# Optimization experiments

Measured on AMD Instinct MI355X. Metric: run time of the kernel, lower is better.

Reference implementation:

```python
import jax, jax.numpy as jnp
import numpy as np

B, S, D = 2, 2048, 1024
H = 16
DH = D // H


def setup_inputs() -> dict:
    key = jax.random.key(0)
    ks = jax.random.split(key, 6)
    scale = 1.0 / np.sqrt(D)
    x = jax.random.normal(ks[0], (B, S, D), dtype=jnp.float32)
    Wq = jax.random.normal(ks[1], (D, D), dtype=jnp.float32) * scale
    Wk = jax.random.normal(ks[2], (D, D), dtype=jnp.float32) * scale
    Wv = jax.random.normal(ks[3], (D, D), dtype=jnp.float32) * scale
    Wo = jax.random.normal(ks[4], (D, D), dtype=jnp.float32) * scale
    bo = jax.random.normal(ks[5], (D,), dtype=jnp.float32) * 0.01
    return {"x": x, "Wq": Wq, "Wk": Wk, "Wv": Wv, "Wo": Wo, "bo": bo}


def reference(x, Wq, Wk, Wv, Wo, bo):
    b, t, _ = x.shape
    # project and split heads: [b, h, t, dh]
    q = (x @ Wq).reshape(b, t, H, DH).transpose(0, 2, 1, 3)
    k = (x @ Wk).reshape(b, t, H, DH).transpose(0, 2, 1, 3)
    v = (x @ Wv).reshape(b, t, H, DH).transpose(0, 2, 1, 3)
    scores = jnp.einsum('bhqd,bhkd->bhqk', q, k)
    causal = jnp.triu(jnp.ones((t, t), dtype=bool), k=1)
    scores = jnp.where(causal, -jnp.inf, scores)
    attn = jax.nn.softmax(scores / np.sqrt(DH), axis=-1)
    ctx = jnp.einsum('bhqk,bhkd->bhqd', attn, v)
    ctx = ctx.transpose(0, 2, 1, 3).reshape(b, t, D)
    return ctx @ Wo + bo
```

## Files before the change

kernel.cpp:

```cpp
#include <hip/hip_runtime.h>
#include <hip/hip_bf16.h>

#define B 2
#define S 2048
#define D 1024
#define NH 16
#define DH 64
#define M (B*S)
#define BQ 128
#define BK 64
#define KSCALE 0.18033688011112042f

typedef __hip_bfloat16 bf16;
typedef __attribute__((ext_vector_type(8))) short frag_ab;
typedef __attribute__((ext_vector_type(4))) float frag_cd;
typedef unsigned long long ull;

__device__ __forceinline__ void gload_lds16(const bf16* g, bf16* l) {
    __builtin_amdgcn_global_load_lds((const __attribute__((address_space(1))) unsigned int*)g,
                                     (__attribute__((address_space(3))) unsigned int*)l,
                                     16, 0, 0);
}

__global__ __launch_bounds__(256) void cvt_x(const float* __restrict__ x, bf16* __restrict__ xb) {
    const int i = (blockIdx.x * 256 + threadIdx.x) * 4;
    const float4 v = *(const float4*)(x + i);
    __align__(8) bf16 t[4] = {__float2bfloat16(v.x), __float2bfloat16(v.y),
                              __float2bfloat16(v.z), __float2bfloat16(v.w)};
    *(ull*)(xb + i) = *(const ull*)t;
}

__global__ __launch_bounds__(256) void cvt_wT(const float* __restrict__ W0, const float* __restrict__ W1,
                                              const float* __restrict__ W2, const float* __restrict__ W3,
                                              bf16* __restrict__ T0, bf16* __restrict__ T1,
                                              bf16* __restrict__ T2, bf16* __restrict__ T3) {
    const float* src; bf16* dst;
    switch (blockIdx.z) {
        case 0: src = W0; dst = T0; break;
        case 1: src = W1; dst = T1; break;
        case 2: src = W2; dst = T2; break;
        default: src = W3; dst = T3; break;
    }
    __shared__ float t[32][33];
    const int tx = threadIdx.x & 31, ty = threadIdx.x >> 5;
    const int c0 = blockIdx.x * 32, r0 = blockIdx.y * 32;
#pragma unroll
    for (int i = 0; i < 4; i++)
        t[ty + 8 * i][tx] = src[(size_t)(r0 + ty + 8 * i) * D + c0 + tx];
    __syncthreads();
#pragma unroll
    for (int i = 0; i < 4; i++)
        dst[(size_t)(c0 + ty + 8 * i) * D + r0 + tx] = __float2bfloat16(t[tx][ty + 8 * i]);
}

__global__ __launch_bounds__(256) void gemm_qkv_all(const bf16* __restrict__ A, const bf16* __restrict__ Bt,
                                                    bf16* __restrict__ Qb, bf16* __restrict__ Kb,
                                                    bf16* __restrict__ Vt_g) {
    __shared__ __align__(16) bf16 As[128 * BK];
    __shared__ __align__(16) bf16 Bs[128 * BK];
    const int tid = threadIdx.x, wave = tid >> 6, lane = tid & 63;
    const int r16 = lane & 15, quad = lane >> 4;
    const int row0 = blockIdx.y * 128;
    const int col0 = blockIdx.x * 128;
    const int wm = (wave & 1) * 64, wn = (wave >> 1) * 64;

    frag_cd acc[4][4];
#pragma unroll
    for (int mt = 0; mt < 4; mt++)
#pragma unroll
        for (int nt = 0; nt < 4; nt++) acc[mt][nt] = frag_cd{0.f, 0.f, 0.f, 0.f};

    for (int k0 = 0; k0 < D; k0 += BK) {
        __syncthreads();
#pragma unroll
        for (int j = 0; j < 4; j++) {
            const int s = wave * 256 + j * 64 + lane;
            const int r = s >> 3;
            const int c = (s ^ r) & 7;
            gload_lds16(A  + (size_t)(row0 + r) * D + k0 + c * 8, &As[(wave * 256 + j * 64) * 8]);
            gload_lds16(Bt + (size_t)(col0 + r) * D + k0 + c * 8, &Bs[(wave * 256 + j * 64) * 8]);
        }
        __syncthreads();

        frag_ab af[4][2], bf[4][2];
#pragma unroll
        for (int mt = 0; mt < 4; mt++) {
            const int row = wm + mt * 16 + r16;
#pragma unroll
            for (int ks = 0; ks < 2; ks++)
                af[mt][ks] = *(const frag_ab*)&As[row * 64 + (((ks * 4 + quad) ^ (row & 7)) * 8)];
        }
#pragma unroll
        for (int nt = 0; nt < 4; nt++) {
            const int row = wn + nt * 16 + r16;
#pragma unroll
            for (int ks = 0; ks < 2; ks++)
                bf[nt][ks] = *(const frag_ab*)&Bs[row * 64 + (((ks * 4 + quad) ^ (row & 7)) * 8)];
        }
#pragma unroll
        for (int mt = 0; mt < 4; mt++)
#pragma unroll
            for (int nt = 0; nt < 4; nt++)
#pragma unroll
                for (int ks = 0; ks < 2; ks++)
                    acc[mt][nt] = __builtin_amdgcn_mfma_f32_16x16x32_bf16(
                        af[mt][ks], bf[nt][ks], acc[mt][nt], 0, 0, 0);
    }

    const int third = col0 >> 10;
    if (third < 2) {
        bf16* Out = (third == 0) ? Qb : Kb;
#pragma unroll
        for (int mt = 0; mt < 4; mt++)
#pragma unroll
            for (int nt = 0; nt < 4; nt++) {
                const int cl = (col0 + wn + nt * 16 + r16) & 1023;
#pragma unroll
                for (int rg = 0; rg < 4; rg++) {
                    const int row = row0 + wm + mt * 16 + quad * 4 + rg;
                    Out[(size_t)row * D + cl] = __float2bfloat16(acc[mt][nt][rg]);
                }
            }
    } else {
        const int bb = row0 >> 11;
        const int sb0 = (row0 & 2047) + wm;
#pragma unroll
        for (int mt = 0; mt < 4; mt++)
#pragma unroll
            for (int nt = 0; nt < 4; nt++) {
                const int c  = (col0 + wn + nt * 16 + r16) - 2048;
                const int hh = c >> 6, dl = c & 63;
                const int sb = sb0 + mt * 16 + quad * 4;
                __align__(8) bf16 t4[4];
#pragma unroll
                for (int rg = 0; rg < 4; rg++) t4[rg] = __float2bfloat16(acc[mt][nt][rg]);
                *(ull*)(Vt_g + (((size_t)bb * 16 + hh) * 64 + dl) * S + sb) = *(const ull*)t4;
            }
    }
}

__global__ __launch_bounds__(256) void attn_mfma(const bf16* __restrict__ Q,
                                                 const bf16* __restrict__ K,
                                                 const bf16* __restrict__ Vg,
                                                 bf16* __restrict__ Ctx) {
    __shared__ __align__(16) bf16 Ks[2][BK * DH];
    __shared__ __align__(16) bf16 Vt[2][BK * DH];
    __shared__ __align__(16) bf16 Qs[BQ * DH];
    bf16* Ps = Qs;

    const int tid = threadIdx.x, wave = tid >> 6, lane = tid & 63;
    const int r16 = lane & 15, quad = lane >> 4;
    const int bh = blockIdx.x, jy = blockIdx.y;
    const int qt = (jy < 8) ? jy : 23 - jy;
    const int b = bh >> 4, h = bh & 15;
    const size_t base  = (size_t)b * S * D + (size_t)h * DH;
    const size_t vbase = (size_t)bh * DH * S;
    const int q0 = qt * BQ;
    const int qwave = q0 + wave * 32;
    const int nkt = 2 * qt + 2;

#pragma unroll
    for (int j = 0; j < 4; j++) {
        const int s = wave * 256 + j * 64 + lane;
        const int r = s >> 3;
        const int c = (s ^ r) & 7;
        gload_lds16(Q + base + (size_t)(q0 + r) * D + c * 8, &Qs[(wave * 256 + j * 64) * 8]);
    }
#pragma unroll
    for (int j = 0; j < 2; j++) {
        const int s = wave * 128 + j * 64 + lane;
        const int r = s >> 3;
        const int c = (s ^ r) & 7;
        gload_lds16(K  + base  + (size_t)r * D + c * 8, &Ks[0][(wave * 128 + j * 64) * 8]);
        gload_lds16(Vg + vbase + (size_t)r * S + c * 8, &Vt[0][(wave * 128 + j * 64) * 8]);
    }
    __syncthreads();

    frag_ab qf[2][2];
#pragma unroll
    for (int nq = 0; nq < 2; nq++)
#pragma unroll
        for (int ks = 0; ks < 2; ks++) {
            const int row = wave * 32 + nq * 16 + r16;
            qf[nq][ks] = *(const frag_ab*)&Qs[row * 64 + (((ks * 4 + quad) ^ (row & 7)) * 8)];
        }

    float mrun[2] = {-1e30f, -1e30f}, lrun[2] = {0.f, 0.f};
    frag_cd Oacc[2][4];
#pragma unroll
    for (int mq = 0; mq < 2; mq++)
#pragma unroll
        for (int nd = 0; nd < 4; nd++) Oacc[mq][nd] = frag_cd{0.f, 0.f, 0.f, 0.f};

    for (int kt = 0; kt < nkt; kt++) {
        const int k0  = kt * BK;
        const int cur = kt & 1;

        if (kt + 1 < nkt) {
            const int kn = k0 + BK;
#pragma unroll
            for (int j = 0; j < 2; j++) {
                const int s = wave * 128 + j * 64 + lane;
                const int r = s >> 3;
                const int c = (s ^ r) & 7;
                gload_lds16(K  + base  + (size_t)(kn + r) * D + c * 8,
                            &Ks[cur ^ 1][(wave * 128 + j * 64) * 8]);
                gload_lds16(Vg + vbase + (size_t)r * S + kn + c * 8,
                            &Vt[cur ^ 1][(wave * 128 + j * 64) * 8]);
            }
        }

        if (k0 <= qwave + 31) {
            frag_ab ka[4][2];
#pragma unroll
            for (int mk = 0; mk < 4; mk++) {
                const int row = mk * 16 + r16;
#pragma unroll
                for (int ks = 0; ks < 2; ks++)
                    ka[mk][ks] = *(const frag_ab*)&Ks[cur][row * 64 + (((ks * 4 + quad) ^ (row & 7)) * 8)];
            }
            const bool domask = (k0 + BK - 1 > qwave);

#pragma unroll
            for (int nq = 0; nq < 2; nq++) {
                frag_cd Sc[4];
#pragma unroll
                for (int mk = 0; mk < 4; mk++) {
                    Sc[mk] = frag_cd{0.f, 0.f, 0.f, 0.f};
#pragma unroll
                    for (int ks = 0; ks < 2; ks++)
                        Sc[mk] = __builtin_amdgcn_mfma_f32_16x16x32_bf16(
                            ka[mk][ks], qf[nq][ks], Sc[mk], 0, 0, 0);
                }
                const int qg = q0 + wave * 32 + nq * 16 + r16;
                float mx = -1e30f;
#pragma unroll
                for (int mk = 0; mk < 4; mk++)
#pragma unroll
                    for (int rg = 0; rg < 4; rg++) {
                        float sv = Sc[mk][rg] * KSCALE;
                        if (domask) {
                            const int keyg = k0 + mk * 16 + quad * 4 + rg;
                            sv = (keyg <= qg) ? sv : -1e30f;
                        }
                        Sc[mk][rg] = sv;
                        mx = fmaxf(mx, sv);
                    }
                mx = fmaxf(mx, __shfl_xor(mx, 16, 64));
                mx = fmaxf(mx, __shfl_xor(mx, 32, 64));
                const float mnew  = fmaxf(mrun[nq], mx);
                const float alpha = __builtin_amdgcn_exp2f(mrun[nq] - mnew);
                mrun[nq] = mnew;
                float rs = 0.f;
#pragma unroll
                for (int mk = 0; mk < 4; mk++)
#pragma unroll
                    for (int rg = 0; rg < 4; rg++) {
                        const float p = __builtin_amdgcn_exp2f(Sc[mk][rg] - mnew);
                        Sc[mk][rg] = p;
                        rs += p;
                    }
                rs += __shfl_xor(rs, 16, 64);
                rs += __shfl_xor(rs, 32, 64);
                lrun[nq] = lrun[nq] * alpha + rs;

                const int qrow = wave * 32 + nq * 16 + r16;
#pragma unroll
                for (int mk = 0; mk < 4; mk++) {
                    __align__(8) bf16 t4[4];
#pragma unroll
                    for (int rg = 0; rg < 4; rg++) t4[rg] = __float2bfloat16(Sc[mk][rg]);
                    const int g = (mk * 4 + quad) ^ r16;
                    *(ull*)&Ps[qrow * 64 + g * 4] = *(const ull*)t4;
                }
#pragma unroll
                for (int nd = 0; nd < 4; nd++)
#pragma unroll
                    for (int rg = 0; rg < 4; rg++) Oacc[nq][nd][rg] *= alpha;
            }

            frag_ab pa[2][2], vb[4][2];
#pragma unroll
            for (int mq = 0; mq < 2; mq++) {
                const int row = wave * 32 + mq * 16 + r16;
#pragma unroll
                for (int ks = 0; ks < 2; ks++) {
                    const int gb = ks * 8 + quad * 2;
                    union { ull u[2]; frag_ab f; } t;
                    t.u[0] = *(const ull*)&Ps[row * 64 + ((gb    ) ^ r16) * 4];
                    t.u[1] = *(const ull*)&Ps[row * 64 + ((gb + 1) ^ r16) * 4];
                    pa[mq][ks] = t.f;
                }
            }
#pragma unroll
            for (int nd = 0; nd < 4; nd++) {
                const int row = nd * 16 + r16;
#pragma unroll
                for (int ks = 0; ks < 2; ks++)
                    vb[nd][ks] = *(const frag_ab*)&Vt[cur][row * 64 + (((ks * 4 + quad) ^ (row & 7)) * 8)];
            }
#pragma unroll
            for (int mq = 0; mq < 2; mq++)
#pragma unroll
                for (int nd = 0; nd < 4; nd++)
#pragma unroll
                    for (int ks = 0; ks < 2; ks++)
                        Oacc[mq][nd] = __builtin_amdgcn_mfma_f32_16x16x32_bf16(
                            vb[nd][ks], pa[mq][ks], Oacc[mq][nd], 0, 0, 0);
        }

        __syncthreads();
    }

#pragma unroll
    for (int mq = 0; mq < 2; mq++) {
        const float invl = 1.f / lrun[mq];
        const int qg = q0 + wave * 32 + mq * 16 + r16;
#pragma unroll
        for (int nd = 0; nd < 4; nd++) {
            __align__(8) bf16 t4[4];
#pragma unroll
            for (int rg = 0; rg < 4; rg++)
                t4[rg] = __float2bfloat16(Oacc[mq][nd][rg] * invl);
            *(ull*)(Ctx + base + (size_t)qg * D + nd * 16 + quad * 4) = *(const ull*)t4;
        }
    }
}

__global__ __launch_bounds__(256) void gemm_out64(const bf16* __restrict__ A, const bf16* __restrict__ Bt,
                                                  const float* __restrict__ bias, float* __restrict__ Out) {
    __shared__ __align__(16) bf16 As[64 * BK];
    __shared__ __align__(16) bf16 Bs[128 * BK];
    const int tid = threadIdx.x, wave = tid >> 6, lane = tid & 63;
    const int r16 = lane & 15, quad = lane >> 4;
    const int row0 = blockIdx.y * 64;
    const int col0 = blockIdx.x * 128;
    const int wm = (wave & 1) * 32, wn = (wave >> 1) * 64;

    frag_cd acc[2][4];
#pragma unroll
    for (int mt = 0; mt < 2; mt++)
#pragma unroll
        for (int nt = 0; nt < 4; nt++) acc[mt][nt] = frag_cd{0.f, 0.f, 0.f, 0.f};

    for (int k0 = 0; k0 < D; k0 += BK) {
        __syncthreads();
#pragma unroll
        for (int j = 0; j < 2; j++) {
            const int s = wave * 128 + j * 64 + lane;
            const int r = s >> 3;
            const int c = (s ^ r) & 7;
            gload_lds16(A + (size_t)(row0 + r) * D + k0 + c * 8, &As[(wave * 128 + j * 64) * 8]);
        }
#pragma unroll
        for (int j = 0; j < 4; j++) {
            const int s = wave * 256 + j * 64 + lane;
            const int r = s >> 3;
            const int c = (s ^ r) & 7;
            gload_lds16(Bt + (size_t)(col0 + r) * D + k0 + c * 8, &Bs[(wave * 256 + j * 64) * 8]);
        }
        __syncthreads();

        frag_ab af[2][2], bf[4][2];
#pragma unroll
        for (int mt = 0; mt < 2; mt++) {
            const int row = wm + mt * 16 + r16;
#pragma unroll
            for (int ks = 0; ks < 2; ks++)
                af[mt][ks] = *(const frag_ab*)&As[row * 64 + (((ks * 4 + quad) ^ (row & 7)) * 8)];
        }
#pragma unroll
        for (int nt = 0; nt < 4; nt++) {
            const int row = wn + nt * 16 + r16;
#pragma unroll
            for (int ks = 0; ks < 2; ks++)
                bf[nt][ks] = *(const frag_ab*)&Bs[row * 64 + (((ks * 4 + quad) ^ (row & 7)) * 8)];
        }
#pragma unroll
        for (int mt = 0; mt < 2; mt++)
#pragma unroll
            for (int nt = 0; nt < 4; nt++)
#pragma unroll
                for (int ks = 0; ks < 2; ks++)
                    acc[mt][nt] = __builtin_amdgcn_mfma_f32_16x16x32_bf16(
                        af[mt][ks], bf[nt][ks], acc[mt][nt], 0, 0, 0);
    }

#pragma unroll
    for (int mt = 0; mt < 2; mt++)
#pragma unroll
        for (int nt = 0; nt < 4; nt++) {
            const int col = col0 + wn + nt * 16 + r16;
            const float bv = bias[col];
#pragma unroll
            for (int rg = 0; rg < 4; rg++) {
                const int row = row0 + wm + mt * 16 + quad * 4 + rg;
                Out[(size_t)row * D + col] = acc[mt][nt][rg] + bv;
            }
        }
}

extern "C" void kernel_launch(void* const* d_in, const int* in_sizes, int n_in,
                              void* d_out, int out_size, void* d_ws, size_t ws_size,
                              hipStream_t stream) {
    const float* x  = (const float*)d_in[0];
    const float* Wq = (const float*)d_in[1];
    const float* Wk = (const float*)d_in[2];
    const float* Wv = (const float*)d_in[3];
    const float* Wo = (const float*)d_in[4];
    const float* bo = (const float*)d_in[5];
    float* out = (float*)d_out;

    bf16* xb    = (bf16*)d_ws;
    bf16* WqkvT = xb    + (size_t)M * D;
    bf16* WoT   = WqkvT + (size_t)3 * D * D;
    bf16* Qb    = WoT   + (size_t)D * D;
    bf16* Kb    = Qb    + (size_t)M * D;
    bf16* Vt_g  = Kb    + (size_t)M * D;
    bf16* Ctxb  = Vt_g  + (size_t)M * D;

    cvt_x<<<(M * D) / 1024, 256, 0, stream>>>(x, xb);
    cvt_wT<<<dim3(32, 32, 4), 256, 0, stream>>>(Wq, Wk, Wv, Wo,
                                                WqkvT, WqkvT + (size_t)D * D,
                                                WqkvT + (size_t)2 * D * D, WoT);
    gemm_qkv_all<<<dim3(24, 32), 256, 0, stream>>>(xb, WqkvT, Qb, Kb, Vt_g);
    attn_mfma<<<dim3(B * NH, S / BQ), 256, 0, stream>>>(Qb, Kb, Vt_g, Ctxb);
    gemm_out64<<<dim3(8, 64), 256, 0, stream>>>(Ctxb, WoT, bo, out);
}
```

Measured before the change: 187.5 us.

## Process key tiles in pairs per barrier and fold softmax scale into Q

The attention loop now stages two 64-key K/V tiles per double-buffer slot and processes both before each barrier and prefetch, halving the number of __syncthreads and prefetch rounds. The softmax scale (including the log2e factor) is applied to Q in the projection epilogue, which removes a per-score multiply from the attention inner loop. LDS use per block rises to about 80KB, which may lower the number of resident blocks per CU. Pre-scaling Q before bf16 rounding also shifts rounding slightly.

```diff
diff --git a/kernel.cpp b/kernel.cpp
--- a/kernel.cpp
+++ b/kernel.cpp
@@ -110,6 +110,7 @@
     const int third = col0 >> 10;
     if (third < 2) {
         bf16* Out = (third == 0) ? Qb : Kb;
+        const float sc = (third == 0) ? KSCALE : 1.f;
 #pragma unroll
         for (int mt = 0; mt < 4; mt++)
 #pragma unroll
@@ -118,7 +119,7 @@
 #pragma unroll
                 for (int rg = 0; rg < 4; rg++) {
                     const int row = row0 + wm + mt * 16 + quad * 4 + rg;
-                    Out[(size_t)row * D + cl] = __float2bfloat16(acc[mt][nt][rg]);
+                    Out[(size_t)row * D + cl] = __float2bfloat16(acc[mt][nt][rg] * sc);
                 }
             }
     } else {
@@ -143,8 +144,8 @@
                                                  const bf16* __restrict__ K,
                                                  const bf16* __restrict__ Vg,
                                                  bf16* __restrict__ Ctx) {
-    __shared__ __align__(16) bf16 Ks[2][BK * DH];
-    __shared__ __align__(16) bf16 Vt[2][BK * DH];
+    __shared__ __align__(16) bf16 Ks[2][2][BK * DH];
+    __shared__ __align__(16) bf16 Vt[2][2][BK * DH];
     __shared__ __align__(16) bf16 Qs[BQ * DH];
     bf16* Ps = Qs;
 
@@ -157,7 +158,7 @@
     const size_t vbase = (size_t)bh * DH * S;
     const int q0 = qt * BQ;
     const int qwave = q0 + wave * 32;
-    const int nkt = 2 * qt + 2;
+    const int npair = qt + 1;
 
 #pragma unroll
     for (int j = 0; j < 4; j++) {
@@ -171,8 +172,13 @@
         const int s = wave * 128 + j * 64 + lane;
         const int r = s >> 3;
         const int c = (s ^ r) & 7;
-        gload_lds16(K  + base  + (size_t)r * D + c * 8, &Ks[0][(wave * 128 + j * 64) * 8]);
-        gload_lds16(Vg + vbase + (size_t)r * S + c * 8, &Vt[0][(wave * 128 + j * 64) * 8]);
+#pragma unroll
+        for (int sub = 0; sub < 2; sub++) {
+            gload_lds16(K  + base  + (size_t)(sub * 64 + r) * D + c * 8,
+                        &Ks[0][sub][(wave * 128 + j * 64) * 8]);
+            gload_lds16(Vg + vbase + (size_t)r * S + sub * 64 + c * 8,
+                        &Vt[0][sub][(wave * 128 + j * 64) * 8]);
+        }
     }
     __syncthreads();
 
@@ -192,32 +198,38 @@
 #pragma unroll
         for (int nd = 0; nd < 4; nd++) Oacc[mq][nd] = frag_cd{0.f, 0.f, 0.f, 0.f};
 
-    for (int kt = 0; kt < nkt; kt++) {
-        const int k0  = kt * BK;
-        const int cur = kt & 1;
-
-        if (kt + 1 < nkt) {
-            const int kn = k0 + BK;
+    for (int p = 0; p < npair; p++) {
+        const int cur = p & 1;
+
+        if (p + 1 < npair) {
+            const int kn = (2 * p + 2) * BK;
 #pragma unroll
             for (int j = 0; j < 2; j++) {
                 const int s = wave * 128 + j * 64 + lane;
                 const int r = s >> 3;
                 const int c = (s ^ r) & 7;
-                gload_lds16(K  + base  + (size_t)(kn + r) * D + c * 8,
-                            &Ks[cur ^ 1][(wave * 128 + j * 64) * 8]);
-                gload_lds16(Vg + vbase + (size_t)r * S + kn + c * 8,
-                            &Vt[cur ^ 1][(wave * 128 + j * 64) * 8]);
-            }
-        }
-
-        if (k0 <= qwave + 31) {
+#pragma unroll
+                for (int sub = 0; sub < 2; sub++) {
+                    gload_lds16(K  + base  + (size_t)(kn + sub * 64 + r) * D + c * 8,
+                                &Ks[cur ^ 1][sub][(wave * 128 + j * 64) * 8]);
+                    gload_lds16(Vg + vbase + (size_t)r * S + kn + sub * 64 + c * 8,
+                                &Vt[cur ^ 1][sub][(wave * 128 + j * 64) * 8]);
+                }
+            }
+        }
+
+#pragma unroll
+        for (int sub = 0; sub < 2; sub++) {
+            const int k0 = (2 * p + sub) * BK;
+            if (k0 > qwave + 31) continue;
+
             frag_ab ka[4][2];
 #pragma unroll
             for (int mk = 0; mk < 4; mk++) {
                 const int row = mk * 16 + r16;
 #pragma unroll
                 for (int ks = 0; ks < 2; ks++)
-                    ka[mk][ks] = *(const frag_ab*)&Ks[cur][row * 64 + (((ks * 4 + quad) ^ (row & 7)) * 8)];
+                    ka[mk][ks] = *(const frag_ab*)&Ks[cur][sub][row * 64 + (((ks * 4 + quad) ^ (row & 7)) * 8)];
             }
             const bool domask = (k0 + BK - 1 > qwave);
 
@@ -238,7 +250,7 @@
                 for (int mk = 0; mk < 4; mk++)
 #pragma unroll
                     for (int rg = 0; rg < 4; rg++) {
-                        float sv = Sc[mk][rg] * KSCALE;
+                        float sv = Sc[mk][rg];
                         if (domask) {
                             const int keyg = k0 + mk * 16 + quad * 4 + rg;
                             sv = (keyg <= qg) ? sv : -1e30f;
@@ -256,9 +268,9 @@
                 for (int mk = 0; mk < 4; mk++)
 #pragma unroll
                     for (int rg = 0; rg < 4; rg++) {
-                        const float p = __builtin_amdgcn_exp2f(Sc[mk][rg] - mnew);
-                        Sc[mk][rg] = p;
-                        rs += p;
+                        const float pv = __builtin_amdgcn_exp2f(Sc[mk][rg] - mnew);
+                        Sc[mk][rg] = pv;
+                        rs += pv;
                     }
                 rs += __shfl_xor(rs, 16, 64);
                 rs += __shfl_xor(rs, 32, 64);
@@ -297,7 +309,7 @@
                 const int row = nd * 16 + r16;
 #pragma unroll
                 for (int ks = 0; ks < 2; ks++)
-                    vb[nd][ks] = *(const frag_ab*)&Vt[cur][row * 64 + (((ks * 4 + quad) ^ (row & 7)) * 8)];
+                    vb[nd][ks] = *(const frag_ab*)&Vt[cur][sub][row * 64 + (((ks * 4 + quad) ^ (row & 7)) * 8)];
             }
 #pragma unroll
             for (int mq = 0; mq < 2; mq++)
```

Measured after the change: 186.7 us. No clear change (-0.4%).

## Double-buffer LDS in both GEMMs, shrink QKV tile, fold softmax scale into Q

Applied to the files above, without the earlier changes.

Both projection GEMMs now use double-buffered LDS tiles, so the next K-slice is fetched while MFMAs run on the current one, with a single barrier per iteration. The QKV GEMM tile drops from 128x128 to 64x128, doubling its grid to give more blocks for the GPU's CUs. The attention score scale is applied once when Q is written, removing a multiply per score in the attention inner loop. The costs are twice the LDS per GEMM block, fewer MFMAs per loaded byte in the QKV GEMM, and rounding of the pre-scaled Q to bf16.

```diff
diff --git a/kernel.cpp b/kernel.cpp
--- a/kernel.cpp
+++ b/kernel.cpp
@@ -56,76 +56,101 @@
 __global__ __launch_bounds__(256) void gemm_qkv_all(const bf16* __restrict__ A, const bf16* __restrict__ Bt,
                                                     bf16* __restrict__ Qb, bf16* __restrict__ Kb,
                                                     bf16* __restrict__ Vt_g) {
-    __shared__ __align__(16) bf16 As[128 * BK];
-    __shared__ __align__(16) bf16 Bs[128 * BK];
+    __shared__ __align__(16) bf16 As[2][64 * BK];
+    __shared__ __align__(16) bf16 Bs[2][128 * BK];
     const int tid = threadIdx.x, wave = tid >> 6, lane = tid & 63;
     const int r16 = lane & 15, quad = lane >> 4;
-    const int row0 = blockIdx.y * 128;
+    const int row0 = blockIdx.y * 64;
     const int col0 = blockIdx.x * 128;
-    const int wm = (wave & 1) * 64, wn = (wave >> 1) * 64;
-
-    frag_cd acc[4][4];
-#pragma unroll
-    for (int mt = 0; mt < 4; mt++)
+    const int wm = (wave & 1) * 32, wn = (wave >> 1) * 64;
+
+    frag_cd acc[2][4];
+#pragma unroll
+    for (int mt = 0; mt < 2; mt++)
 #pragma unroll
         for (int nt = 0; nt < 4; nt++) acc[mt][nt] = frag_cd{0.f, 0.f, 0.f, 0.f};
 
-    for (int k0 = 0; k0 < D; k0 += BK) {
-        __syncthreads();
-#pragma unroll
-        for (int j = 0; j < 4; j++) {
-            const int s = wave * 256 + j * 64 + lane;
-            const int r = s >> 3;
-            const int c = (s ^ r) & 7;
-            gload_lds16(A  + (size_t)(row0 + r) * D + k0 + c * 8, &As[(wave * 256 + j * 64) * 8]);
-            gload_lds16(Bt + (size_t)(col0 + r) * D + k0 + c * 8, &Bs[(wave * 256 + j * 64) * 8]);
-        }
-        __syncthreads();
-
-        frag_ab af[4][2], bf[4][2];
-#pragma unroll
-        for (int mt = 0; mt < 4; mt++) {
+#pragma unroll
+    for (int j = 0; j < 2; j++) {
+        const int s = wave * 128 + j * 64 + lane;
+        const int r = s >> 3, c = (s ^ r) & 7;
+        gload_lds16(A + (size_t)(row0 + r) * D + c * 8, &As[0][(wave * 128 + j * 64) * 8]);
+    }
+#pragma unroll
+    for (int j = 0; j < 4; j++) {
+        const int s = wave * 256 + j * 64 + lane;
+        const int r = s >> 3, c = (s ^ r) & 7;
+        gload_lds16(Bt + (size_t)(col0 + r) * D + c * 8, &Bs[0][(wave * 256 + j * 64) * 8]);
+    }
+    __syncthreads();
+
+    for (int kt = 0; kt < D / BK; kt++) {
+        const int cur = kt & 1;
+        if (kt + 1 < D / BK) {
+            const int kn = (kt + 1) * BK;
+#pragma unroll
+            for (int j = 0; j < 2; j++) {
+                const int s = wave * 128 + j * 64 + lane;
+                const int r = s >> 3, c = (s ^ r) & 7;
+                gload_lds16(A + (size_t)(row0 + r) * D + kn + c * 8,
+                            &As[cur ^ 1][(wave * 128 + j * 64) * 8]);
+            }
+#pragma unroll
+            for (int j = 0; j < 4; j++) {
+                const int s = wave * 256 + j * 64 + lane;
+                const int r = s >> 3, c = (s ^ r) & 7;
+                gload_lds16(Bt + (size_t)(col0 + r) * D + kn + c * 8,
+                            &Bs[cur ^ 1][(wave * 256 + j * 64) * 8]);
+            }
+        }
+
+        frag_ab af[2][2], bf[4][2];
+#pragma unroll
+        for (int mt = 0; mt < 2; mt++) {
             const int row = wm + mt * 16 + r16;
 #pragma unroll
             for (int ks = 0; ks < 2; ks++)
-                af[mt][ks] = *(const frag_ab*)&As[row * 64 + (((ks * 4 + quad) ^ (row & 7)) * 8)];
+                af[mt][ks] = *(const frag_ab*)&As[cur][row * 64 + (((ks * 4 + quad) ^ (row & 7)) * 8)];
         }
 #pragma unroll
         for (int nt = 0; nt < 4; nt++) {
             const int row = wn + nt * 16 + r16;
 #pragma unroll
             for (int ks = 0; ks < 2; ks++)
-                bf[nt][ks] = *(const frag_ab*)&Bs[row * 64 + (((ks * 4 + quad) ^ (row & 7)) * 8)];
-        }
-#pragma unroll
-        for (int mt = 0; mt < 4; mt++)
+                bf[nt][ks] = *(const frag_ab*)&Bs[cur][row * 64 + (((ks * 4 + quad) ^ (row & 7)) * 8)];
+        }
+#pragma unroll
+        for (int mt = 0; mt < 2; mt++)
 #pragma unroll
             for (int nt = 0; nt < 4; nt++)
 #pragma unroll
                 for (int ks = 0; ks < 2; ks++)
                     acc[mt][nt] = __builtin_amdgcn_mfma_f32_16x16x32_bf16(
                         af[mt][ks], bf[nt][ks], acc[mt][nt], 0, 0, 0);
+
+        __syncthreads();
     }
 
     const int third = col0 >> 10;
     if (third < 2) {
         bf16* Out = (third == 0) ? Qb : Kb;
-#pragma unroll
-        for (int mt = 0; mt < 4; mt++)
+        const float sc = (third == 0) ? KSCALE : 1.f;
+#pragma unroll
+        for (int mt = 0; mt < 2; mt++)
 #pragma unroll
             for (int nt = 0; nt < 4; nt++) {
                 const int cl = (col0 + wn + nt * 16 + r16) & 1023;
 #pragma unroll
                 for (int rg = 0; rg < 4; rg++) {
                     const int row = row0 + wm + mt * 16 + quad * 4 + rg;
-                    Out[(size_t)row * D + cl] = __float2bfloat16(acc[mt][nt][rg]);
+                    Out[(size_t)row * D + cl] = __float2bfloat16(acc[mt][nt][rg] * sc);
                 }
             }
     } else {
         const int bb = row0 >> 11;
         const int sb0 = (row0 & 2047) + wm;
 #pragma unroll
-        for (int mt = 0; mt < 4; mt++)
+        for (int mt = 0; mt < 2; mt++)
 #pragma unroll
             for (int nt = 0; nt < 4; nt++) {
                 const int c  = (col0 + wn + nt * 16 + r16) - 2048;
@@ -162,15 +187,13 @@
 #pragma unroll
     for (int j = 0; j < 4; j++) {
         const int s = wave * 256 + j * 64 + lane;
-        const int r = s >> 3;
-        const int c = (s ^ r) & 7;
+        const int r = s >> 3, c = (s ^ r) & 7;
         gload_lds16(Q + base + (size_t)(q0 + r) * D + c * 8, &Qs[(wave * 256 + j * 64) * 8]);
     }
 #pragma unroll
     for (int j = 0; j < 2; j++) {
         const int s = wave * 128 + j * 64 + lane;
-        const int r = s >> 3;
-        const int c = (s ^ r) & 7;
+        const int r = s >> 3, c = (s ^ r) & 7;
         gload_lds16(K  + base  + (size_t)r * D + c * 8, &Ks[0][(wave * 128 + j * 64) * 8]);
         gload_lds16(Vg + vbase + (size_t)r * S + c * 8, &Vt[0][(wave * 128 + j * 64) * 8]);
     }
@@ -201,8 +224,7 @@
 #pragma unroll
             for (int j = 0; j < 2; j++) {
                 const int s = wave * 128 + j * 64 + lane;
-                const int r = s >> 3;
-                const int c = (s ^ r) & 7;
+                const int r = s >> 3, c = (s ^ r) & 7;
                 gload_lds16(K  + base  + (size_t)(kn + r) * D + c * 8,
                             &Ks[cur ^ 1][(wave * 128 + j * 64) * 8]);
                 gload_lds16(Vg + vbase + (size_t)r * S + kn + c * 8,
@@ -238,7 +260,7 @@
                 for (int mk = 0; mk < 4; mk++)
 #pragma unroll
                     for (int rg = 0; rg < 4; rg++) {
-                        float sv = Sc[mk][rg] * KSCALE;
+                        float sv = Sc[mk][rg];
                         if (domask) {
                             const int keyg = k0 + mk * 16 + quad * 4 + rg;
                             sv = (keyg <= qg) ? sv : -1e30f;
@@ -256,9 +278,9 @@
                 for (int mk = 0; mk < 4; mk++)
 #pragma unroll
                     for (int rg = 0; rg < 4; rg++) {
-                        const float p = __builtin_amdgcn_exp2f(Sc[mk][rg] - mnew);
-                        Sc[mk][rg] = p;
-                        rs += p;
+                        const float pv = __builtin_amdgcn_exp2f(Sc[mk][rg] - mnew);
+                        Sc[mk][rg] = pv;
+                        rs += pv;
                     }
                 rs += __shfl_xor(rs, 16, 64);
                 rs += __shfl_xor(rs, 32, 64);
@@ -329,8 +351,8 @@
 
 __global__ __launch_bounds__(256) void gemm_out64(const bf16* __restrict__ A, const bf16* __restrict__ Bt,
                                                   const float* __restrict__ bias, float* __restrict__ Out) {
-    __shared__ __align__(16) bf16 As[64 * BK];
-    __shared__ __align__(16) bf16 Bs[128 * BK];
+    __shared__ __align__(16) bf16 As[2][64 * BK];
+    __shared__ __align__(16) bf16 Bs[2][128 * BK];
     const int tid = threadIdx.x, wave = tid >> 6, lane = tid & 63;
     const int r16 = lane & 15, quad = lane >> 4;
     const int row0 = blockIdx.y * 64;
@@ -343,23 +365,39 @@
 #pragma unroll
         for (int nt = 0; nt < 4; nt++) acc[mt][nt] = frag_cd{0.f, 0.f, 0.f, 0.f};
 
-    for (int k0 = 0; k0 < D; k0 += BK) {
-        __syncthreads();
-#pragma unroll
-        for (int j = 0; j < 2; j++) {
-            const int s = wave * 128 + j * 64 + lane;
-            const int r = s >> 3;
-            const int c = (s ^ r) & 7;
-            gload_lds16(A + (size_t)(row0 + r) * D + k0 + c * 8, &As[(wave * 128 + j * 64) * 8]);
-        }
-#pragma unroll
-        for (int j = 0; j < 4; j++) {
-            const int s = wave * 256 + j * 64 + lane;
-            const int r = s >> 3;
-            const int c = (s ^ r) & 7;
-            gload_lds16(Bt + (size_t)(col0 + r) * D + k0 + c * 8, &Bs[(wave * 256 + j * 64) * 8]);
-        }
-        __syncthreads();
+#pragma unroll
+    for (int j = 0; j < 2; j++) {
+        const int s = wave * 128 + j * 64 + lane;
+        const int r = s >> 3, c = (s ^ r) & 7;
+        gload_lds16(A + (size_t)(row0 + r) * D + c * 8, &As[0][(wave * 128 + j * 64) * 8]);
+    }
+#pragma unroll
+    for (int j = 0; j < 4; j++) {
+        const int s = wave * 256 + j * 64 + lane;
+        const int r = s >> 3, c = (s ^ r) & 7;
+        gload_lds16(Bt + (size_t)(col0 + r) * D + c * 8, &Bs[0][(wave * 256 + j * 64) * 8]);
+    }
+    __syncthreads();
+
+    for (int kt = 0; kt < D / BK; kt++) {
+        const int cur = kt & 1;
+        if (kt + 1 < D / BK) {
+            const int kn = (kt + 1) * BK;
+#pragma unroll
+            for (int j = 0; j < 2; j++) {
+                const int s = wave * 128 + j * 64 + lane;
+                const int r = s >> 3, c = (s ^ r) & 7;
+                gload_lds16(A + (size_t)(row0 + r) * D + kn + c * 8,
+                            &As[cur ^ 1][(wave * 128 + j * 64) * 8]);
+            }
+#pragma unroll
+            for (int j = 0; j < 4; j++) {
+                const int s = wave * 256 + j * 64 + lane;
+                const int r = s >> 3, c = (s ^ r) & 7;
+                gload_lds16(Bt + (size_t)(col0 + r) * D + kn + c * 8,
+                            &Bs[cur ^ 1][(wave * 256 + j * 64) * 8]);
+            }
+        }
 
         frag_ab af[2][2], bf[4][2];
 #pragma unroll
@@ -367,14 +405,14 @@
             const int row = wm + mt * 16 + r16;
 #pragma unroll
             for (int ks = 0; ks < 2; ks++)
-                af[mt][ks] = *(const frag_ab*)&As[row * 64 + (((ks * 4 + quad) ^ (row & 7)) * 8)];
+                af[mt][ks] = *(const frag_ab*)&As[cur][row * 64 + (((ks * 4 + quad) ^ (row & 7)) * 8)];
         }
 #pragma unroll
         for (int nt = 0; nt < 4; nt++) {
             const int row = wn + nt * 16 + r16;
 #pragma unroll
             for (int ks = 0; ks < 2; ks++)
-                bf[nt][ks] = *(const frag_ab*)&Bs[row * 64 + (((ks * 4 + quad) ^ (row & 7)) * 8)];
+                bf[nt][ks] = *(const frag_ab*)&Bs[cur][row * 64 + (((ks * 4 + quad) ^ (row & 7)) * 8)];
         }
 #pragma unroll
         for (int mt = 0; mt < 2; mt++)
@@ -384,6 +422,8 @@
                 for (int ks = 0; ks < 2; ks++)
                     acc[mt][nt] = __builtin_amdgcn_mfma_f32_16x16x32_bf16(
                         af[mt][ks], bf[nt][ks], acc[mt][nt], 0, 0, 0);
+
+        __syncthreads();
     }
 
 #pragma unroll
@@ -423,7 +463,7 @@
     cvt_wT<<<dim3(32, 32, 4), 256, 0, stream>>>(Wq, Wk, Wv, Wo,
                                                 WqkvT, WqkvT + (size_t)D * D,
                                                 WqkvT + (size_t)2 * D * D, WoT);
-    gemm_qkv_all<<<dim3(24, 32), 256, 0, stream>>>(xb, WqkvT, Qb, Kb, Vt_g);
+    gemm_qkv_all<<<dim3(24, 64), 256, 0, stream>>>(xb, WqkvT, Qb, Kb, Vt_g);
     attn_mfma<<<dim3(B * NH, S / BQ), 256, 0, stream>>>(Qb, Kb, Vt_g, Ctxb);
     gemm_out64<<<dim3(8, 64), 256, 0, stream>>>(Ctxb, WoT, bo, out);
 }
```

New measurement: 199.3 us. +6.3%, slower.

## Halve attention query tile to 64 rows and fold softmax scale into Q

Applied to the files above, without the earlier changes.

Shrinks the attention query tile from 128 to 64 rows, so each wave owns 16 query rows instead of 32. This doubles the number of blocks and cuts per-wave register state, which should help occupancy and load balance across CUs. The softmax scale is now applied to Q in the projection epilogue, removing a multiply per score element. The cost is that each K/V tile is reused by half as many queries, so K/V traffic per query rises; the launch grid presumably also changes in hidden code.

```diff
diff --git a/kernel.cpp b/kernel.cpp
--- a/kernel.cpp
+++ b/kernel.cpp
@@ -7,7 +7,7 @@
 #define NH 16
 #define DH 64
 #define M (B*S)
-#define BQ 128
+#define BQ 64
 #define BK 64
 #define KSCALE 0.18033688011112042f
 
@@ -110,6 +110,7 @@
     const int third = col0 >> 10;
     if (third < 2) {
         bf16* Out = (third == 0) ? Qb : Kb;
+        const float sc = (third == 0) ? KSCALE : 1.f;
 #pragma unroll
         for (int mt = 0; mt < 4; mt++)
 #pragma unroll
@@ -118,7 +119,7 @@
 #pragma unroll
                 for (int rg = 0; rg < 4; rg++) {
                     const int row = row0 + wm + mt * 16 + quad * 4 + rg;
-                    Out[(size_t)row * D + cl] = __float2bfloat16(acc[mt][nt][rg]);
+                    Out[(size_t)row * D + cl] = __float2bfloat16(acc[mt][nt][rg] * sc);
                 }
             }
     } else {
@@ -151,46 +152,41 @@
     const int tid = threadIdx.x, wave = tid >> 6, lane = tid & 63;
     const int r16 = lane & 15, quad = lane >> 4;
     const int bh = blockIdx.x, jy = blockIdx.y;
-    const int qt = (jy < 8) ? jy : 23 - jy;
+    const int qt = (jy < 16) ? jy : 47 - jy;
     const int b = bh >> 4, h = bh & 15;
     const size_t base  = (size_t)b * S * D + (size_t)h * DH;
     const size_t vbase = (size_t)bh * DH * S;
     const int q0 = qt * BQ;
-    const int qwave = q0 + wave * 32;
-    const int nkt = 2 * qt + 2;
-
-#pragma unroll
-    for (int j = 0; j < 4; j++) {
-        const int s = wave * 256 + j * 64 + lane;
-        const int r = s >> 3;
-        const int c = (s ^ r) & 7;
-        gload_lds16(Q + base + (size_t)(q0 + r) * D + c * 8, &Qs[(wave * 256 + j * 64) * 8]);
-    }
+    const int qwave = q0 + wave * 16;
+    const int nkt = qt + 1;
+
 #pragma unroll
     for (int j = 0; j < 2; j++) {
         const int s = wave * 128 + j * 64 + lane;
-        const int r = s >> 3;
-        const int c = (s ^ r) & 7;
+        const int r = s >> 3, c = (s ^ r) & 7;
+        gload_lds16(Q + base + (size_t)(q0 + r) * D + c * 8, &Qs[(wave * 128 + j * 64) * 8]);
+    }
+#pragma unroll
+    for (int j = 0; j < 2; j++) {
+        const int s = wave * 128 + j * 64 + lane;
+        const int r = s >> 3, c = (s ^ r) & 7;
         gload_lds16(K  + base  + (size_t)r * D + c * 8, &Ks[0][(wave * 128 + j * 64) * 8]);
         gload_lds16(Vg + vbase + (size_t)r * S + c * 8, &Vt[0][(wave * 128 + j * 64) * 8]);
     }
     __syncthreads();
 
-    frag_ab qf[2][2];
-#pragma unroll
-    for (int nq = 0; nq < 2; nq++)
-#pragma unroll
-        for (int ks = 0; ks < 2; ks++) {
-            const int row = wave * 32 + nq * 16 + r16;
-            qf[nq][ks] = *(const frag_ab*)&Qs[row * 64 + (((ks * 4 + quad) ^ (row & 7)) * 8)];
-        }
-
-    float mrun[2] = {-1e30f, -1e30f}, lrun[2] = {0.f, 0.f};
-    frag_cd Oacc[2][4];
-#pragma unroll
-    for (int mq = 0; mq < 2; mq++)
-#pragma unroll
-        for (int nd = 0; nd < 4; nd++) Oacc[mq][nd] = frag_cd{0.f, 0.f, 0.f, 0.f};
+    frag_ab qf[2];
+    {
+        const int row = wave * 16 + r16;
+#pragma unroll
+        for (int ks = 0; ks < 2; ks++)
+            qf[ks] = *(const frag_ab*)&Qs[row * 64 + (((ks * 4 + quad) ^ (row & 7)) * 8)];
+    }
+
+    float mrun = -1e30f, lrun = 0.f;
+    frag_cd Oacc[4];
+#pragma unroll
+    for (int nd = 0; nd < 4; nd++) Oacc[nd] = frag_cd{0.f, 0.f, 0.f, 0.f};
 
     for (int kt = 0; kt < nkt; kt++) {
         const int k0  = kt * BK;
@@ -201,8 +197,7 @@
 #pragma unroll
             for (int j = 0; j < 2; j++) {
                 const int s = wave * 128 + j * 64 + lane;
-                const int r = s >> 3;
-                const int c = (s ^ r) & 7;
+                const int r = s >> 3, c = (s ^ r) & 7;
                 gload_lds16(K  + base  + (size_t)(kn + r) * D + c * 8,
                             &Ks[cur ^ 1][(wave * 128 + j * 64) * 8]);
                 gload_lds16(Vg + vbase + (size_t)r * S + kn + c * 8,
@@ -210,7 +205,7 @@
             }
         }
 
-        if (k0 <= qwave + 31) {
+        if (k0 <= qwave + 15) {
             frag_ab ka[4][2];
 #pragma unroll
             for (int mk = 0; mk < 4; mk++) {
@@ -221,76 +216,70 @@
             }
             const bool domask = (k0 + BK - 1 > qwave);
 
-#pragma unroll
-            for (int nq = 0; nq < 2; nq++) {
-                frag_cd Sc[4];
-#pragma unroll
-                for (int mk = 0; mk < 4; mk++) {
-                    Sc[mk] = frag_cd{0.f, 0.f, 0.f, 0.f};
-#pragma unroll
-                    for (int ks = 0; ks < 2; ks++)
-                        Sc[mk] = __builtin_amdgcn_mfma_f32_16x16x32_bf16(
-                            ka[mk][ks], qf[nq][ks], Sc[mk], 0, 0, 0);
+            frag_cd Sc[4];
+#pragma unroll
+            for (int mk = 0; mk < 4; mk++) {
+                Sc[mk] = frag_cd{0.f, 0.f, 0.f, 0.f};
+#pragma unroll
+                for (int ks = 0; ks < 2; ks++)
+                    Sc[mk] = __builtin_amdgcn_mfma_f32_16x16x32_bf16(
+                        ka[mk][ks], qf[ks], Sc[mk], 0, 0, 0);
+            }
+            const int qg = qwave + r16;
+            float mx = -1e30f;
+#pragma unroll
+            for (int mk = 0; mk < 4; mk++)
+#pragma unroll
+                for (int rg = 0; rg < 4; rg++) {
+                    float sv = Sc[mk][rg];
+                    if (domask) {
+                        const int keyg = k0 + mk * 16 + quad * 4 + rg;
+                        sv = (keyg <= qg) ? sv : -1e30f;
+                    }
+                    Sc[mk][rg] = sv;
+                    mx = fmaxf(mx, sv);
                 }
-                const int qg = q0 + wave * 32 + nq * 16 + r16;
-                float mx = -1e30f;
-#pragma unroll
-                for (int mk = 0; mk < 4; mk++)
-#pragma unroll
-                    for (int rg = 0; rg < 4; rg++) {
-                        float sv = Sc[mk][rg] * KSCALE;
-                        if (domask) {
-                            const int keyg = k0 + mk * 16 + quad * 4 + rg;
-                            sv = (keyg <= qg) ? sv : -1e30f;
-                        }
-                        Sc[mk][rg] = sv;
-                        mx = fmaxf(mx, sv);
-                    }
-                mx = fmaxf(mx, __shfl_xor(mx, 16, 64));
-                mx = fmaxf(mx, __shfl_xor(mx, 32, 64));
-                const float mnew  = fmaxf(mrun[nq], mx);
-                const float alpha = __builtin_amdgcn_exp2f(mrun[nq] - mnew);
-                mrun[nq] = mnew;
-                float rs = 0.f;
-#pragma unroll
-                for (int mk = 0; mk < 4; mk++)
-#pragma unroll
-                    for (int rg = 0; rg < 4; rg++) {
-                        const float p = __builtin_amdgcn_exp2f(Sc[mk][rg] - mnew);
-                        Sc[mk][rg] = p;
-                        rs += p;
-                    }
-                rs += __shfl_xor(rs, 16, 64);
-                rs += __shfl_xor(rs, 32, 64);
-                lrun[nq] = lrun[nq] * alpha + rs;
-
-                const int qrow = wave * 32 + nq * 16 + r16;
-#pragma unroll
-                for (int mk = 0; mk < 4; mk++) {
-                    __align__(8) bf16 t4[4];
-#pragma unroll
-                    for (int rg = 0; rg < 4; rg++) t4[rg] = __float2bfloat16(Sc[mk][rg]);
-                    const int g = (mk * 4 + quad) ^ r16;
-                    *(ull*)&Ps[qrow * 64 + g * 4] = *(const ull*)t4;
+            mx = fmaxf(mx, __shfl_xor(mx, 16, 64));
+            mx = fmaxf(mx, __shfl_xor(mx, 32, 64));
+            const float mnew  = fmaxf(mrun, mx);
+            const float alpha = __builtin_amdgcn_exp2f(mrun - mnew);
+            mrun = mnew;
+            float rs = 0.f;
+#pragma unroll
+            for (int mk = 0; mk < 4; mk++)
+#pragma unroll
+                for (int rg = 0; rg < 4; rg++) {
+                    const float pv = __builtin_amdgcn_exp2f(Sc[mk][rg] - mnew);
+                    Sc[mk][rg] = pv;
+                    rs += pv;
                 }
-#pragma unroll
-                for (int nd = 0; nd < 4; nd++)
-#pragma unroll
-                    for (int rg = 0; rg < 4; rg++) Oacc[nq][nd][rg] *= alpha;
-            }
-
-            frag_ab pa[2][2], vb[4][2];
-#pragma unroll
-            for (int mq = 0; mq < 2; mq++) {
-                const int row = wave * 32 + mq * 16 + r16;
-#pragma unroll
-                for (int ks = 0; ks < 2; ks++) {
-                    const int gb = ks * 8 + quad * 2;
-                    union { ull u[2]; frag_ab f; } t;
-                    t.u[0] = *(const ull*)&Ps[row * 64 + ((gb    ) ^ r16) * 4];
-                    t.u[1] = *(const ull*)&Ps[row * 64 + ((gb + 1) ^ r16) * 4];
-                    pa[mq][ks] = t.f;
-                }
+            rs += __shfl_xor(rs, 16, 64);
+            rs += __shfl_xor(rs, 32, 64);
+            lrun = lrun * alpha + rs;
+
+            const int qrow = wave * 16 + r16;
+#pragma unroll
+            for (int mk = 0; mk < 4; mk++) {
+                __align__(8) bf16 t4[4];
+#pragma unroll
+                for (int rg = 0; rg < 4; rg++) t4[rg] = __float2bfloat16(Sc[mk][rg]);
+                const int g = (mk * 4 + quad) ^ r16;
+                *(ull*)&Ps[qrow * 64 + g * 4] = *(const ull*)t4;
+            }
+#pragma unroll
+            for (int nd = 0; nd < 4; nd++)
+#pragma unroll
+                for (int rg = 0; rg < 4; rg++) Oacc[nd][rg] *= alpha;
+
+
+            frag_ab pa[2], vb[4][2];
+#pragma unroll
+            for (int ks = 0; ks < 2; ks++) {
+                const int gb = ks * 8 + quad * 2;
+                union { ull u[2]; frag_ab f; } t;
+                t.u[0] = *(const ull*)&Ps[qrow * 64 + ((gb    ) ^ r16) * 4];
+                t.u[1] = *(const ull*)&Ps[qrow * 64 + ((gb + 1) ^ r16) * 4];
+                pa[ks] = t.f;
             }
 #pragma unroll
             for (int nd = 0; nd < 4; nd++) {
@@ -300,28 +289,25 @@
                     vb[nd][ks] = *(const frag_ab*)&Vt[cur][row * 64 + (((ks * 4 + quad) ^ (row & 7)) * 8)];
             }
 #pragma unroll
-            for (int mq = 0; mq < 2; mq++)
-#pragma unroll
-                for (int nd = 0; nd < 4; nd++)
-#pragma unroll
-                    for (int ks = 0; ks < 2; ks++)
-                        Oacc[mq][nd] = __builtin_amdgcn_mfma_f32_16x16x32_bf16(
-                            vb[nd][ks], pa[mq][ks], Oacc[mq][nd], 0, 0, 0);
+            for (int nd = 0; nd < 4; nd++)
+#pragma unroll
+                for (int ks = 0; ks < 2; ks++)
+                    Oacc[nd] = __builtin_amdgcn_mfma_f32_16x16x32_bf16(
+                        vb[nd][ks], pa[ks], Oacc[nd], 0, 0, 0);
         }
 
         __syncthreads();
     }
 
-#pragma unroll
-    for (int mq = 0; mq < 2; mq++) {
-        const float invl = 1.f / lrun[mq];
-        const int qg = q0 + wave * 32 + mq * 16 + r16;
+    {
+        const float invl = 1.f / lrun;
+        const int qg = qwave + r16;
 #pragma unroll
         for (int nd = 0; nd < 4; nd++) {
             __align__(8) bf16 t4[4];
 #pragma unroll
             for (int rg = 0; rg < 4; rg++)
-                t4[rg] = __float2bfloat16(Oacc[mq][nd][rg] * invl);
+                t4[rg] = __float2bfloat16(Oacc[nd][rg] * invl);
             *(ull*)(Ctx + base + (size_t)qg * D + nd * 16 + quad * 4) = *(const ull*)t4;
         }
     }
@@ -348,15 +334,13 @@
 #pragma unroll
         for (int j = 0; j < 2; j++) {
             const int s = wave * 128 + j * 64 + lane;
-            const int r = s >> 3;
-            const int c = (s ^ r) & 7;
+            const int r = s >> 3, c = (s ^ r) & 7;
             gload_lds16(A + (size_t)(row0 + r) * D + k0 + c * 8, &As[(wave * 128 + j * 64) * 8]);
         }
 #pragma unroll
         for (int j = 0; j < 4; j++) {
             const int s = wave * 256 + j * 64 + lane;
-            const int r = s >> 3;
-            const int c = (s ^ r) & 7;
+            const int r = s >> 3, c = (s ^ r) & 7;
             gload_lds16(Bt + (size_t)(col0 + r) * D + k0 + c * 8, &Bs[(wave * 256 + j * 64) * 8]);
         }
         __syncthreads();
```

Measured after the change: 181.0 us. -3.4%, faster.
